# Performance work log

Measured on AMD Instinct MI355X. Metric: run time of the kernel, lower is better.

## Reference

```python
import jax, jax.numpy as jnp
import numpy as np

HID = 128          # hidden_dim
IN_DIM = 256       # input_dim
BOT = 128          # bottleneck_dim
OUT = 4            # output_dim
NQ = 131072        # num query (mesh) points
E = 262144         # num grid->query edges
SEQ = 262144       # grid points (64^3)
B = 1
PE_DIM = 4 * HID   # 512, sincos embed dim over ndim=4


def _linear_params(key, fin, fout):
    k1, k2 = jax.random.split(key)
    lim = 1.0 / np.sqrt(fin)
    w = jax.random.uniform(k1, (fin, fout), minval=-lim, maxval=lim, dtype=jnp.float32)
    b = jax.random.uniform(k2, (fout,), minval=-lim, maxval=lim, dtype=jnp.float32)
    return w, b


def setup_inputs() -> dict:
    key = jax.random.key(0)
    ks = jax.random.split(key, 10)
    x = jax.random.normal(ks[0], (B, SEQ, IN_DIM), dtype=jnp.float32)
    # raw positions in [0, 200) so query_pos/100 - 1 lands in [-1, 1)
    query_pos = jax.random.uniform(ks[1], (NQ, 3), dtype=jnp.float32) * 200.0
    qidx = jnp.sort(jax.random.randint(ks[2], (E,), 0, NQ))          # sorted, as segment_csr assumes
    gidx = jax.random.randint(ks[3], (E,), 0, B * SEQ)
    grid_to_query_edges = jnp.stack([qidx, gidx], axis=1)            # [E, 2] (query_idx, grid_idx)

    msg_w0, msg_b0 = _linear_params(ks[4], IN_DIM + PE_DIM, 512)
    msg_w1, msg_b1 = _linear_params(ks[5], 512, 256)
    msg_w2, msg_b2 = _linear_params(ks[6], 256, BOT)
    pred_w0, pred_b0 = _linear_params(ks[7], BOT, 256)
    pred_w1, pred_b1 = _linear_params(ks[8], 256, OUT)
    return dict(x=x, query_pos=query_pos, grid_to_query_edges=grid_to_query_edges,
                msg_w0=msg_w0, msg_b0=msg_b0, msg_w1=msg_w1, msg_b1=msg_b1,
                msg_w2=msg_w2, msg_b2=msg_b2,
                pred_w0=pred_w0, pred_b0=pred_b0, pred_w1=pred_w1, pred_b1=pred_b1)


def _sincos_embed(coords):
    # coords: [N, 4]; dim=512 -> 128 per coord -> 64 frequencies (no padding needed)
    eff = PE_DIM // 4
    omega = 1.0 / (10000.0 ** (jnp.arange(0, eff, 2, dtype=jnp.float32) / eff))  # [64]
    out = coords[..., None] * omega                                  # [N, 4, 64]
    emb = jnp.concatenate([jnp.sin(out), jnp.cos(out)], axis=-1)     # [N, 4, 128]
    return emb.reshape(coords.shape[0], -1)                          # [N, 512]


def _gelu(x):
    return jax.nn.gelu(x, approximate=False)  # torch nn.GELU default is exact erf


def reference(x, query_pos, grid_to_query_edges,
              msg_w0, msg_b0, msg_w1, msg_b1, msg_w2, msg_b2,
              pred_w0, pred_b0, pred_w1, pred_b1):
    qp = query_pos / 100.0 - 1.0
    ones = jnp.ones((qp.shape[0], 1), dtype=qp.dtype)
    qp = jnp.concatenate([qp, ones], axis=1)                         # [NQ, 4]
    pe = _sincos_embed(qp)                                           # [NQ, 512]

    xf = x.reshape(-1, x.shape[-1])                                  # [B*SEQ, IN_DIM]
    qidx = grid_to_query_edges[:, 0]
    gidx = grid_to_query_edges[:, 1]

    feat = jnp.concatenate([xf[gidx], pe[qidx]], axis=1)             # [E, 768]
    h = _gelu(feat @ msg_w0 + msg_b0)
    h = _gelu(h @ msg_w1 + msg_b1)
    h = h @ msg_w2 + msg_b2                                          # [E, BOT]

    nq = qp.shape[0]
    sums = jax.ops.segment_sum(h, qidx, num_segments=nq)             # [NQ, BOT]
    counts = jax.ops.segment_sum(jnp.ones((h.shape[0],), h.dtype), qidx, num_segments=nq)
    mean = sums / jnp.maximum(counts, 1.0)[:, None]                  # empty segments -> 0 (segment_csr mean)

    out = _gelu(mean @ pred_w0 + pred_b0) @ pred_w1 + pred_b1        # [NQ, OUT]
    return out
```

## Files before the change

kernel.cpp:

```cpp
#include <hip/hip_runtime.h>
#include <cmath>

#define IN_DIM   256
#define H0_DIM   512
#define H1_DIM   256
#define BOT      128
#define NQ_      131072
#define NE_      262144
#define SEQ_     262144
#define QWIN     32768
#define NWIN     (NQ_/QWIN)
#define PE_K     384

static const size_t OFF_XH    = 0;
static const size_t OFF_XL    = 134217728;
static const size_t OFF_Z     = 268435456;
static const size_t OFF_PEH   = 536870912;
static const size_t OFF_PEL   = 562036736;
static const size_t OFF_H2    = 738197504;
static const size_t OFF_W0AH  = 872415232;
static const size_t OFF_W0AL  = 872677376;
static const size_t OFF_W0BH  = 872939520;
static const size_t OFF_W0BL  = 873332736;
static const size_t OFF_W1H   = 873725952;
static const size_t OFF_W1L   = 873988096;
static const size_t OFF_W2H   = 874250240;
static const size_t OFF_W2L   = 874315776;
static const size_t OFF_PW0H  = 874381312;
static const size_t OFF_PW0L  = 874446848;
static const size_t OFF_BCONST= 874512384;
static const size_t OFF_START = 874514432;
static const size_t OFF_MEANH = 0;
static const size_t OFF_MEANL = 33554432;
static const size_t OFF_G1    = 268435456;

typedef __attribute__((ext_vector_type(8))) short bf16x8;
typedef __attribute__((ext_vector_type(4))) float f32x4;

__device__ __forceinline__ float gelu_f(float v) {
    return v * 0.5f * (1.0f + erff(v * 0.7071067811865476f));
}
__device__ __forceinline__ unsigned short f2bf(float f) {
    unsigned int u = __float_as_uint(f);
    unsigned int r = (u + 0x7FFFu + ((u >> 16) & 1u)) >> 16;
    return (unsigned short)r;
}
__device__ __forceinline__ float bf2f(unsigned short h) {
    return __uint_as_float(((unsigned int)h) << 16);
}
__device__ __forceinline__ unsigned int pack2(unsigned short a, unsigned short b) {
    return (unsigned int)a | ((unsigned int)b << 16);
}
__device__ __forceinline__ void stage16(const void* g, void* l) {
    __builtin_amdgcn_global_load_lds(
        (const __attribute__((address_space(1))) unsigned int*)g,
        (__attribute__((address_space(3))) unsigned int*)l,
        16, 0, 0);
}
__device__ __forceinline__ void cvt4(const float4 v, unsigned int* hw, unsigned int* lw) {
    const unsigned short a = f2bf(v.x), b = f2bf(v.y), c = f2bf(v.z), d = f2bf(v.w);
    hw[0] = pack2(a, b); hw[1] = pack2(c, d);
    lw[0] = pack2(f2bf(v.x - bf2f(a)), f2bf(v.y - bf2f(b)));
    lw[1] = pack2(f2bf(v.z - bf2f(c)), f2bf(v.w - bf2f(d)));
}

__global__ __launch_bounds__(256) void conv_x(
    const float* __restrict__ x,
    unsigned short* __restrict__ xH, unsigned short* __restrict__ xL)
{
    const int wv = threadIdx.x >> 6;
    const int l  = threadIdx.x & 63;
    const int row = blockIdx.x * 4 + wv;
    const size_t base = (size_t)row * IN_DIM + l * 4;
    float4 v = *(const float4*)&x[base];
    unsigned short h0 = f2bf(v.x), h1 = f2bf(v.y), h2 = f2bf(v.z), h3 = f2bf(v.w);
    uint2 H, L;
    H.x = pack2(h0, h1); H.y = pack2(h2, h3);
    L.x = pack2(f2bf(v.x - bf2f(h0)), f2bf(v.y - bf2f(h1)));
    L.y = pack2(f2bf(v.z - bf2f(h2)), f2bf(v.w - bf2f(h3)));
    *(uint2*)&xH[base] = H;
    *(uint2*)&xL[base] = L;
}

__global__ __launch_bounds__(256) void conv_w(
    const float* __restrict__ W, unsigned short* __restrict__ WTh,
    unsigned short* __restrict__ WTl, int K, int N)
{
    int idx = blockIdx.x * 256 + threadIdx.x;
    if (idx >= K * N) return;
    int k = idx / N, n = idx % N;
    float v = W[idx];
    unsigned short h = f2bf(v);
    WTh[(size_t)n * K + k] = h;
    WTl[(size_t)n * K + k] = f2bf(v - bf2f(h));
}

__global__ __launch_bounds__(256) void bias_fold(
    const float* __restrict__ w0, const float* __restrict__ b0,
    float* __restrict__ bconst)
{
    int n = blockIdx.x * 256 + threadIdx.x;
    if (n >= H0_DIM) return;
    float s = b0[n];
    for (int j = 0; j < 64; ++j) {
        float om = exp2f((float)j * (-13.287712379549449f / 64.0f));
        s += sinf(om) * w0[(size_t)(640 + j) * H0_DIM + n];
        s += cosf(om) * w0[(size_t)(704 + j) * H0_DIM + n];
    }
    bconst[n] = s;
}

__global__ __launch_bounds__(256) void seg_offsets(
    const int* __restrict__ edges, int* __restrict__ start)
{
    int e = blockIdx.x * 256 + threadIdx.x;
    if (e > NE_) return;
    int qc = (e < NE_) ? edges[2 * e] : NQ_;
    int qp = (e > 0) ? edges[2 * e - 2] : -1;
    for (int q = qp + 1; q <= qc; ++q) start[q] = e;
}

__global__ __launch_bounds__(256) void build_pe(
    const float* __restrict__ qpos, int qbase,
    unsigned short* __restrict__ peH, unsigned short* __restrict__ peL)
{
    const int wv = threadIdx.x >> 6;
    const int l  = threadIdx.x & 63;
    const int i  = blockIdx.x * 4 + wv;
    const int i0 = l * 8;
    if (i0 >= PE_K) return;
    const int q  = qbase + i;
    const size_t base = (size_t)i * PE_K;

    const int cc = i0 >> 7;
    const int j0 = i0 & 127;
    const float cv = qpos[q * 3 + cc] * 0.01f - 1.0f;
    const bool is_sin = (j0 < 64);
    const int jj0 = j0 & 63;
    unsigned int hw[4], lw[4];
    #pragma unroll
    for (int p2 = 0; p2 < 4; ++p2) {
        unsigned short hh[2], ll[2];
        #pragma unroll
        for (int s = 0; s < 2; ++s) {
            int jj = jj0 + p2 * 2 + s;
            float om  = exp2f((float)jj * (-13.287712379549449f / 64.0f));
            float arg = cv * om;
            float v   = is_sin ? __sinf(arg) : __cosf(arg);
            unsigned short h = f2bf(v);
            hh[s] = h; ll[s] = f2bf(v - bf2f(h));
        }
        hw[p2] = pack2(hh[0], hh[1]);
        lw[p2] = pack2(ll[0], ll[1]);
    }
    uint4 H, L;
    H.x = hw[0]; H.y = hw[1]; H.z = hw[2]; H.w = hw[3];
    L.x = lw[0]; L.y = lw[1]; L.z = lw[2]; L.w = lw[3];
    *(uint4*)&peH[base + i0] = H;
    *(uint4*)&peL[base + i0] = L;
}

template <int ACT, int OUT_MODE, int GATHER>
__global__ __launch_bounds__(256) void gemm_mfma(
    const unsigned short* __restrict__ Ah, const unsigned short* __restrict__ Al,
    const unsigned short* __restrict__ Bh, const unsigned short* __restrict__ Bl,
    const float* __restrict__ bias,
    float* __restrict__ Cf, unsigned short* __restrict__ ChO, unsigned short* __restrict__ ClO,
    int M, int K, int N,
    const int* __restrict__ gp, const float* __restrict__ Zw)
{
    __shared__ __align__(16) short lds[4][128][32];

    const int tid = threadIdx.x;
    const int w   = tid >> 6;
    const int l   = tid & 63;
    const int l16 = l & 15;
    const int lq  = l >> 4;
    const int bm  = blockIdx.y * 128;
    const int bn  = blockIdx.x * 128;
    const int wm  = (w & 1) * 64;
    const int wn  = (w >> 1) * 64;

    f32x4 acc[4][4];
    #pragma unroll
    for (int i = 0; i < 4; ++i)
        #pragma unroll
        for (int j = 0; j < 4; ++j)
            acc[i][j] = (f32x4){0.f, 0.f, 0.f, 0.f};

    const int jrow = l >> 2;
    const int jkc  = l & 3;
    const int t0 = w * 2, t1 = t0 + 1;
    const int r0 = t0 * 16 + jrow, r1 = t1 * 16 + jrow;

    size_t arow0, arow1;
    if (GATHER) {
        arow0 = (size_t)gp[2 * (bm + r0) + 1] * K;
        arow1 = (size_t)gp[2 * (bm + r1) + 1] * K;
    } else {
        arow0 = (size_t)(bm + r0) * K;
        arow1 = (size_t)(bm + r1) * K;
    }
    const size_t brow0 = (size_t)(bn + r0) * K;
    const size_t brow1 = (size_t)(bn + r1) * K;
    short* d00 = &lds[0][0][0] + t0 * 512;
    short* d01 = &lds[1][0][0] + t0 * 512;
    short* d02 = &lds[2][0][0] + t0 * 512;
    short* d03 = &lds[3][0][0] + t0 * 512;
    short* d10 = &lds[0][0][0] + t1 * 512;
    short* d11 = &lds[1][0][0] + t1 * 512;
    short* d12 = &lds[2][0][0] + t1 * 512;
    short* d13 = &lds[3][0][0] + t1 * 512;

    for (int k0 = 0; k0 < K; k0 += 32) {
        const int ko = k0 + jkc * 8;
        stage16(Ah + arow0 + ko, d00);
        stage16(Al + arow0 + ko, d01);
        stage16(Bh + brow0 + ko, d02);
        stage16(Bl + brow0 + ko, d03);
        stage16(Ah + arow1 + ko, d10);
        stage16(Al + arow1 + ko, d11);
        stage16(Bh + brow1 + ko, d12);
        stage16(Bl + brow1 + ko, d13);
        __syncthreads();

        bf16x8 ah[4], al[4], bh[4], bl[4];
        #pragma unroll
        for (int i = 0; i < 4; ++i) {
            ah[i] = *(const bf16x8*)&lds[0][wm + i*16 + l16][lq*8];
            al[i] = *(const bf16x8*)&lds[1][wm + i*16 + l16][lq*8];
            bh[i] = *(const bf16x8*)&lds[2][wn + i*16 + l16][lq*8];
            bl[i] = *(const bf16x8*)&lds[3][wn + i*16 + l16][lq*8];
        }
        #pragma unroll
        for (int i = 0; i < 4; ++i)
            #pragma unroll
            for (int j = 0; j < 4; ++j) {
                acc[i][j] = __builtin_amdgcn_mfma_f32_16x16x32_bf16(ah[i], bh[j], acc[i][j], 0, 0, 0);
                acc[i][j] = __builtin_amdgcn_mfma_f32_16x16x32_bf16(ah[i], bl[j], acc[i][j], 0, 0, 0);
                acc[i][j] = __builtin_amdgcn_mfma_f32_16x16x32_bf16(al[i], bh[j], acc[i][j], 0, 0, 0);
            }
        __syncthreads();
    }

    if (OUT_MODE == 0) {
        #pragma unroll
        for (int j = 0; j < 4; ++j) {
            int n = bn + wn + j * 16 + l16;
            float bv = bias[n];
            #pragma unroll
            for (int i = 0; i < 4; ++i) {
                int mrow = bm + wm + i * 16 + lq * 4;
                #pragma unroll
                for (int r = 0; r < 4; ++r) {
                    float v = acc[i][j][r] + bv;
                    if (ACT) v = gelu_f(v);
                    Cf[(size_t)(mrow + r) * N + n] = v;
                }
            }
        }
    }
}

__global__ __launch_bounds__(256, 2) void fused_edge(
    const unsigned short* __restrict__ xHg, const unsigned short* __restrict__ xLg,
    const unsigned short* __restrict__ w0aHg, const unsigned short* __restrict__ w0aLg,
    const unsigned short* __restrict__ w1Hg, const unsigned short* __restrict__ w1Lg,
    const unsigned short* __restrict__ w2Hg, const unsigned short* __restrict__ w2Lg,
    const float* __restrict__ Zg, const float* __restrict__ b1g,
    const float* __restrict__ b2g, const int* __restrict__ gp,
    float* __restrict__ h2g)
{
    extern __shared__ __align__(16) short smem[];
    short* stg = smem;
    short* h0h = smem + 16384;
    short* h0l = smem + 24576;

    const int tid = threadIdx.x;
    const int w   = tid >> 6;
    const int l   = tid & 63;
    const int l16 = l & 15;
    const int lq  = l >> 4;
    const int bm  = blockIdx.x * 64;

    const int wn_p = w * 32;
    const int wn1  = w * 64;

    const int rx = tid >> 2;
    const int ux = tid & 3;
    const size_t xoff = (size_t)gp[2 * (bm + rx) + 1] * IN_DIM + ux * 8;
    const int q_e = gp[2 * (bm + l)];
    float* lbuf = ((float*)stg) + w * 2048;

    short* stgAh  = stg;
    short* stgAl  = stg + 2048;
    short* stgBh  = stg + 4096;
    short* stgBl  = stg + 8192;
    short* stgW1h = stg;
    short* stgW1l = stg + 8192;
    short* stgW2h = stg;
    short* stgW2l = stg + 4096;

    f32x4 h1acc[4][4];
    #pragma unroll
    for (int i = 0; i < 4; ++i)
        #pragma unroll
        for (int j = 0; j < 4; ++j)
            h1acc[i][j] = (f32x4){0.f, 0.f, 0.f, 0.f};

    for (int c = 0; c < 4; ++c) {
        f32x4 acc1[4][2];
        #pragma unroll
        for (int i = 0; i < 4; ++i)
            #pragma unroll
            for (int j = 0; j < 2; ++j)
                acc1[i][j] = (f32x4){0.f, 0.f, 0.f, 0.f};

        {
            const size_t wo = (size_t)(c * 128 + rx) * IN_DIM + ux * 8;
            stage16(xHg + xoff, stgAh + tid * 8);
            stage16(xLg + xoff, stgAl + tid * 8);
            stage16(w0aHg + wo,                      stgBh + tid * 8);
            stage16(w0aLg + wo,                      stgBl + tid * 8);
            stage16(w0aHg + wo + (size_t)64 * IN_DIM, stgBh + 2048 + tid * 8);
            stage16(w0aLg + wo + (size_t)64 * IN_DIM, stgBl + 2048 + tid * 8);
        }
        __syncthreads();
        for (int ks = 0; ks < 8; ++ks) {
            bf16x8 ah[4], al[4], bh[2], bl[2];
            #pragma unroll
            for (int i = 0; i < 4; ++i) {
                const int ro = (i * 16 + l16) * 32 + lq * 8;
                ah[i] = *(const bf16x8*)&stgAh[ro];
                al[i] = *(const bf16x8*)&stgAl[ro];
            }
            #pragma unroll
            for (int j = 0; j < 2; ++j) {
                const int ro = (wn_p + j * 16 + l16) * 32 + lq * 8;
                bh[j] = *(const bf16x8*)&stgBh[ro];
                bl[j] = *(const bf16x8*)&stgBl[ro];
            }
            __syncthreads();
            if (ks < 7) {
                const int ko = (ks + 1) * 32;
                const size_t wo = (size_t)(c * 128 + rx) * IN_DIM + ko + ux * 8;
                stage16(xHg + xoff + ko, stgAh + tid * 8);
                stage16(xLg + xoff + ko, stgAl + tid * 8);
                stage16(w0aHg + wo,                      stgBh + tid * 8);
                stage16(w0aLg + wo,                      stgBl + tid * 8);
                stage16(w0aHg + wo + (size_t)64 * IN_DIM, stgBh + 2048 + tid * 8);
                stage16(w0aLg + wo + (size_t)64 * IN_DIM, stgBl + 2048 + tid * 8);
            }
            #pragma unroll
            for (int i = 0; i < 4; ++i)
                #pragma unroll
                for (int j = 0; j < 2; ++j) {
                    acc1[i][j] = __builtin_amdgcn_mfma_f32_16x16x32_bf16(ah[i], bh[j], acc1[i][j], 0, 0, 0);
                    acc1[i][j] = __builtin_amdgcn_mfma_f32_16x16x32_bf16(ah[i], bl[j], acc1[i][j], 0, 0, 0);
                    acc1[i][j] = __builtin_amdgcn_mfma_f32_16x16x32_bf16(al[i], bh[j], acc1[i][j], 0, 0, 0);
                }
            __syncthreads();
        }

        #pragma unroll
        for (int j = 0; j < 2; ++j)
            #pragma unroll
            for (int i = 0; i < 4; ++i)
                #pragma unroll
                for (int r = 0; r < 4; ++r) {
                    const int rowq = i * 16 + lq * 4 + r;
                    const int u = j * 4 + (l16 >> 2);
                    lbuf[rowq * 32 + (((u ^ (rowq & 7)) << 2) | (l16 & 3))] = acc1[i][j][r];
                }
        __syncthreads();
        {
            const float* zrow = Zg + (size_t)q_e * H0_DIM + c * 128 + wn_p;
            #pragma unroll
            for (int g = 0; g < 2; ++g) {
                unsigned int hw[8], lw[8];
                #pragma unroll
                for (int c2 = 0; c2 < 4; ++c2) {
                    const int cq = g * 4 + c2;
                    float4 v = *(const float4*)&lbuf[l * 32 + ((cq ^ (l & 7)) << 2)];
                    const float4 z = *(const float4*)&zrow[cq * 4];
                    v.x = gelu_f(v.x + z.x); v.y = gelu_f(v.y + z.y);
                    v.z = gelu_f(v.z + z.z); v.w = gelu_f(v.w + z.w);
                    cvt4(v, &hw[c2 * 2], &lw[c2 * 2]);
                }
                const int u0 = (wn_p >> 3) + g * 2;
                const int o0 = l * 128 + (((u0    ) ^ (l & 7)) << 3);
                const int o1 = l * 128 + (((u0 + 1) ^ (l & 7)) << 3);
                uint4 H0, H1, L0, L1;
                H0.x = hw[0]; H0.y = hw[1]; H0.z = hw[2]; H0.w = hw[3];
                H1.x = hw[4]; H1.y = hw[5]; H1.z = hw[6]; H1.w = hw[7];
                L0.x = lw[0]; L0.y = lw[1]; L0.z = lw[2]; L0.w = lw[3];
                L1.x = lw[4]; L1.y = lw[5]; L1.z = lw[6]; L1.w = lw[7];
                *(uint4*)&h0h[o0] = H0; *(uint4*)&h0h[o1] = H1;
                *(uint4*)&h0l[o0] = L0; *(uint4*)&h0l[o1] = L1;
            }
        }
        __syncthreads();

        {
            #pragma unroll
            for (int p = 0; p < 4; ++p) {
                const size_t o = (size_t)(rx + 64 * p) * H0_DIM + c * 128 + ux * 8;
                stage16(w1Hg + o, stgW1h + p * 2048 + tid * 8);
                stage16(w1Lg + o, stgW1l + p * 2048 + tid * 8);
            }
        }
        __syncthreads();
        for (int ks = 0; ks < 4; ++ks) {
            bf16x8 ah[4], al[4], bh[4], bl[4];
            #pragma unroll
            for (int i = 0; i < 4; ++i) {
                const int row = i * 16 + l16;
                const int uo = ((ks * 4 + lq) ^ (row & 7)) << 3;
                ah[i] = *(const bf16x8*)&h0h[row * 128 + uo];
                al[i] = *(const bf16x8*)&h0l[row * 128 + uo];
            }
            #pragma unroll
            for (int j = 0; j < 4; ++j) {
                const int ro = (wn1 + j * 16 + l16) * 32 + lq * 8;
                bh[j] = *(const bf16x8*)&stgW1h[ro];
                bl[j] = *(const bf16x8*)&stgW1l[ro];
            }
            __syncthreads();
            if (ks < 3) {
                #pragma unroll
                for (int p = 0; p < 4; ++p) {
                    const size_t o = (size_t)(rx + 64 * p) * H0_DIM + c * 128 + (ks + 1) * 32 + ux * 8;
                    stage16(w1Hg + o, stgW1h + p * 2048 + tid * 8);
                    stage16(w1Lg + o, stgW1l + p * 2048 + tid * 8);
                }
            }
            #pragma unroll
            for (int i = 0; i < 4; ++i)
                #pragma unroll
                for (int j = 0; j < 4; ++j) {
                    h1acc[i][j] = __builtin_amdgcn_mfma_f32_16x16x32_bf16(ah[i], bh[j], h1acc[i][j], 0, 0, 0);
                    h1acc[i][j] = __builtin_amdgcn_mfma_f32_16x16x32_bf16(ah[i], bl[j], h1acc[i][j], 0, 0, 0);
                    h1acc[i][j] = __builtin_amdgcn_mfma_f32_16x16x32_bf16(al[i], bh[j], h1acc[i][j], 0, 0, 0);
                }
            __syncthreads();
        }
    }

    f32x4 acc2[4][2];
    #pragma unroll
    for (int i = 0; i < 4; ++i)
        #pragma unroll
        for (int j = 0; j < 2; ++j)
            acc2[i][j] = (f32x4){0.f, 0.f, 0.f, 0.f};

    for (int kh = 0; kh < 2; ++kh) {
        const bool my = ((w >> 1) == kh);
        #pragma unroll
        for (int j2 = 0; j2 < 2; ++j2) {
            if (my) {
                #pragma unroll
                for (int jj = 0; jj < 2; ++jj) {
                    const int j = j2 * 2 + jj;
                    const float bv = b1g[wn1 + j * 16 + l16];
                    #pragma unroll
                    for (int i = 0; i < 4; ++i)
                        #pragma unroll
                        for (int r = 0; r < 4; ++r) {
                            const int rowq = i * 16 + lq * 4 + r;
                            const int u = jj * 4 + (l16 >> 2);
                            lbuf[rowq * 32 + (((u ^ (rowq & 7)) << 2) | (l16 & 3))] =
                                gelu_f(h1acc[i][j][r] + bv);
                        }
                }
            }
            __syncthreads();
            if (my) {
                const int colb = (w & 1) * 64 + j2 * 32;
                #pragma unroll
                for (int g = 0; g < 2; ++g) {
                    unsigned int hw[8], lw[8];
                    #pragma unroll
                    for (int c2 = 0; c2 < 4; ++c2) {
                        const int cq = g * 4 + c2;
                        float4 v = *(const float4*)&lbuf[l * 32 + ((cq ^ (l & 7)) << 2)];
                        cvt4(v, &hw[c2 * 2], &lw[c2 * 2]);
                    }
                    const int u0 = ((colb + g * 16) >> 3);
                    const int o0 = l * 128 + (((u0    ) ^ (l & 7)) << 3);
                    const int o1 = l * 128 + (((u0 + 1) ^ (l & 7)) << 3);
                    uint4 H0, H1, L0, L1;
                    H0.x = hw[0]; H0.y = hw[1]; H0.z = hw[2]; H0.w = hw[3];
                    H1.x = hw[4]; H1.y = hw[5]; H1.z = hw[6]; H1.w = hw[7];
                    L0.x = lw[0]; L0.y = lw[1]; L0.z = lw[2]; L0.w = lw[3];
                    L1.x = lw[4]; L1.y = lw[5]; L1.z = lw[6]; L1.w = lw[7];
                    *(uint4*)&h0h[o0] = H0; *(uint4*)&h0h[o1] = H1;
                    *(uint4*)&h0l[o0] = L0; *(uint4*)&h0l[o1] = L1;
                }
            }
            __syncthreads();
        }

        {
            #pragma unroll
            for (int p = 0; p < 2; ++p) {
                const size_t o = (size_t)(rx + 64 * p) * H1_DIM + kh * 128 + ux * 8;
                stage16(w2Hg + o, stgW2h + p * 2048 + tid * 8);
                stage16(w2Lg + o, stgW2l + p * 2048 + tid * 8);
            }
        }
        __syncthreads();
        for (int ks = 0; ks < 4; ++ks) {
            bf16x8 ah[4], al[4], bh[2], bl[2];
            #pragma unroll
            for (int i = 0; i < 4; ++i) {
                const int row = i * 16 + l16;
                const int uo = ((ks * 4 + lq) ^ (row & 7)) << 3;
                ah[i] = *(const bf16x8*)&h0h[row * 128 + uo];
                al[i] = *(const bf16x8*)&h0l[row * 128 + uo];
            }
            #pragma unroll
            for (int j = 0; j < 2; ++j) {
                const int ro = (wn_p + j * 16 + l16) * 32 + lq * 8;
                bh[j] = *(const bf16x8*)&stgW2h[ro];
                bl[j] = *(const bf16x8*)&stgW2l[ro];
            }
            __syncthreads();
            if (ks < 3) {
                #pragma unroll
                for (int p = 0; p < 2; ++p) {
                    const size_t o = (size_t)(rx + 64 * p) * H1_DIM + kh * 128 + (ks + 1) * 32 + ux * 8;
                    stage16(w2Hg + o, stgW2h + p * 2048 + tid * 8);
                    stage16(w2Lg + o, stgW2l + p * 2048 + tid * 8);
                }
            }
            #pragma unroll
            for (int i = 0; i < 4; ++i)
                #pragma unroll
                for (int j = 0; j < 2; ++j) {
                    acc2[i][j] = __builtin_amdgcn_mfma_f32_16x16x32_bf16(ah[i], bh[j], acc2[i][j], 0, 0, 0);
                    acc2[i][j] = __builtin_amdgcn_mfma_f32_16x16x32_bf16(ah[i], bl[j], acc2[i][j], 0, 0, 0);
                    acc2[i][j] = __builtin_amdgcn_mfma_f32_16x16x32_bf16(al[i], bh[j], acc2[i][j], 0, 0, 0);
                }
            __syncthreads();
        }
    }

    #pragma unroll
    for (int j = 0; j < 2; ++j) {
        const int n = wn_p + j * 16 + l16;
        const float bv = b2g[n];
        #pragma unroll
        for (int i = 0; i < 4; ++i) {
            const int er = bm + i * 16 + lq * 4;
            #pragma unroll
            for (int r = 0; r < 4; ++r)
                h2g[(size_t)(er + r) * BOT + n] = acc2[i][j][r] + bv;
        }
    }
}

__global__ __launch_bounds__(256) void seg_mean(
    const int* __restrict__ start, const float* __restrict__ h2,
    unsigned short* __restrict__ mH, unsigned short* __restrict__ mL)
{
    const int t = threadIdx.x;
    const int q = blockIdx.x * 8 + (t >> 5);
    const int quad = t & 31;
    const int s = start[q];
    const int e = start[q + 1];

    float4 acc = make_float4(0.f, 0.f, 0.f, 0.f);
    for (int i = s; i < e; ++i) {
        const float4 v = *(const float4*)&h2[(size_t)i * BOT + quad * 4];
        acc.x += v.x; acc.y += v.y; acc.z += v.z; acc.w += v.w;
    }
    const float inv = 1.0f / (float)((e - s) > 0 ? (e - s) : 1);
    float m0 = acc.x * inv, m1 = acc.y * inv, m2 = acc.z * inv, m3 = acc.w * inv;
    unsigned short h0 = f2bf(m0), h1 = f2bf(m1), h2s = f2bf(m2), h3 = f2bf(m3);
    uint2 H, L;
    H.x = pack2(h0, h1); H.y = pack2(h2s, h3);
    L.x = pack2(f2bf(m0 - bf2f(h0)), f2bf(m1 - bf2f(h1)));
    L.y = pack2(f2bf(m2 - bf2f(h2s)), f2bf(m3 - bf2f(h3)));
    *(uint2*)&mH[(size_t)q * BOT + quad * 4] = H;
    *(uint2*)&mL[(size_t)q * BOT + quad * 4] = L;
}

__global__ __launch_bounds__(256) void pred1_kernel(
    const float* __restrict__ g1, const float* __restrict__ w,
    const float* __restrict__ b, float* __restrict__ out)
{
    const int wave = threadIdx.x >> 6;
    const int lane = threadIdx.x & 63;
    const int row  = blockIdx.x * 4 + wave;

    const float* g = g1 + (size_t)row * 256;
    float a0 = 0, a1 = 0, a2 = 0, a3 = 0;
    #pragma unroll
    for (int i = 0; i < 4; ++i) {
        int k = lane + 64 * i;
        float gv = g[k];
        const float* wr = w + k * 4;
        a0 = fmaf(gv, wr[0], a0);
        a1 = fmaf(gv, wr[1], a1);
        a2 = fmaf(gv, wr[2], a2);
        a3 = fmaf(gv, wr[3], a3);
    }
    #pragma unroll
    for (int off = 32; off > 0; off >>= 1) {
        a0 += __shfl_down(a0, off, 64);
        a1 += __shfl_down(a1, off, 64);
        a2 += __shfl_down(a2, off, 64);
        a3 += __shfl_down(a3, off, 64);
    }
    if (lane == 0) {
        float4 o = {a0 + b[0], a1 + b[1], a2 + b[2], a3 + b[3]};
        *(float4*)&out[(size_t)row * 4] = o;
    }
}

extern "C" void kernel_launch(void* const* d_in, const int* in_sizes, int n_in,
                              void* d_out, int out_size, void* d_ws, size_t ws_size,
                              hipStream_t stream)
{
    const float* x    = (const float*)d_in[0];
    const float* qpos = (const float*)d_in[1];
    const int*   edges= (const int*)  d_in[2];
    const float* w0   = (const float*)d_in[3];
    const float* b0   = (const float*)d_in[4];
    const float* w1   = (const float*)d_in[5];
    const float* b1   = (const float*)d_in[6];
    const float* w2   = (const float*)d_in[7];
    const float* b2   = (const float*)d_in[8];
    const float* pw0  = (const float*)d_in[9];
    const float* pb0  = (const float*)d_in[10];
    const float* pw1  = (const float*)d_in[11];
    const float* pb1  = (const float*)d_in[12];
    float* out = (float*)d_out;

    char* ws = (char*)d_ws;
    unsigned short* xH    = (unsigned short*)(ws + OFF_XH);
    unsigned short* xL    = (unsigned short*)(ws + OFF_XL);
    float*          Z     = (float*)(ws + OFF_Z);
    unsigned short* peH   = (unsigned short*)(ws + OFF_PEH);
    unsigned short* peL   = (unsigned short*)(ws + OFF_PEL);
    float*          h2    = (float*)(ws + OFF_H2);
    unsigned short* w0aH  = (unsigned short*)(ws + OFF_W0AH);
    unsigned short* w0aL  = (unsigned short*)(ws + OFF_W0AL);
    unsigned short* w0bH  = (unsigned short*)(ws + OFF_W0BH);
    unsigned short* w0bL  = (unsigned short*)(ws + OFF_W0BL);
    unsigned short* w1H   = (unsigned short*)(ws + OFF_W1H);
    unsigned short* w1L   = (unsigned short*)(ws + OFF_W1L);
    unsigned short* w2H   = (unsigned short*)(ws + OFF_W2H);
    unsigned short* w2L   = (unsigned short*)(ws + OFF_W2L);
    unsigned short* pw0H  = (unsigned short*)(ws + OFF_PW0H);
    unsigned short* pw0L  = (unsigned short*)(ws + OFF_PW0L);
    float*          bconst= (float*)(ws + OFF_BCONST);
    int*            start = (int*)(ws + OFF_START);
    unsigned short* meanH = (unsigned short*)(ws + OFF_MEANH);
    unsigned short* meanL = (unsigned short*)(ws + OFF_MEANL);
    float*          g1    = (float*)(ws + OFF_G1);

    static bool attr_done = false;
    if (!attr_done) {
        hipFuncSetAttribute(reinterpret_cast<const void*>(&fused_edge),
                            hipFuncAttributeMaxDynamicSharedMemorySize, 65536);
        attr_done = true;
    }

    conv_x<<<SEQ_/4, 256, 0, stream>>>(x, xH, xL);
    conv_w<<<(IN_DIM*H0_DIM + 255)/256, 256, 0, stream>>>(w0, w0aH, w0aL, IN_DIM, H0_DIM);
    conv_w<<<(PE_K*H0_DIM + 255)/256, 256, 0, stream>>>(w0 + (size_t)IN_DIM*H0_DIM, w0bH, w0bL, PE_K, H0_DIM);
    conv_w<<<(H0_DIM*H1_DIM + 255)/256, 256, 0, stream>>>(w1, w1H, w1L, H0_DIM, H1_DIM);
    conv_w<<<(H1_DIM*BOT + 255)/256, 256, 0, stream>>>(w2, w2H, w2L, H1_DIM, BOT);
    conv_w<<<(BOT*H1_DIM + 255)/256, 256, 0, stream>>>(pw0, pw0H, pw0L, BOT, H1_DIM);
    bias_fold<<<2, 256, 0, stream>>>(w0, b0, bconst);
    seg_offsets<<<(NE_ + 1 + 255)/256, 256, 0, stream>>>(edges, start);

    for (int wn = 0; wn < NWIN; ++wn) {
        build_pe<<<QWIN/4, 256, 0, stream>>>(qpos, wn * QWIN, peH, peL);
        gemm_mfma<0, 0, 0><<<dim3(H0_DIM/128, QWIN/128), 256, 0, stream>>>(
            peH, peL, w0bH, w0bL, bconst, Z + (size_t)wn * QWIN * H0_DIM,
            nullptr, nullptr, QWIN, PE_K, H0_DIM, nullptr, nullptr);
    }

    fused_edge<<<NE_/64, 256, 65536, stream>>>(
        xH, xL, w0aH, w0aL, w1H, w1L, w2H, w2L,
        Z, b1, b2, edges, h2);

    seg_mean<<<NQ_/8, 256, 0, stream>>>(start, h2, meanH, meanL);
    gemm_mfma<1, 0, 0><<<dim3(H1_DIM/128, NQ_/128), 256, 0, stream>>>(
        meanH, meanL, pw0H, pw0L, pb0, g1, nullptr, nullptr,
        NQ_, BOT, H1_DIM, nullptr, nullptr);
    pred1_kernel<<<NQ_/4, 256, 0, stream>>>(g1, pw1, pb1, out);
}
```

Measured before the change: 1.580 ms.

## Double-buffer LDS staging with XOR swizzle in GEMM and fused edge kernel

Converts the k-loop staging in gemm_mfma and the first layer of fused_edge to a two-buffer pipeline. Loads for step k+2 are issued while step k computes, and explicit vmcnt/lgkmcnt waits replace full syncthreads. It also XOR-swizzles the LDS column chunk to reduce bank conflicts on the bf16x8 reads. The cost is more LDS (fused_edge dynamic shared memory grows to 80KB), which could reduce occupancy, and the hand-written waitcnt logic is fragile.

```diff
diff --git a/kernel.cpp b/kernel.cpp
--- a/kernel.cpp
+++ b/kernel.cpp
@@ -57,6 +57,11 @@
         (__attribute__((address_space(3))) unsigned int*)l,
         16, 0, 0);
 }
+#define WAITV0 asm volatile("s_waitcnt vmcnt(0)" ::: "memory")
+#define WAITV6 asm volatile("s_waitcnt vmcnt(6)" ::: "memory")
+#define WAITV8 asm volatile("s_waitcnt vmcnt(8)" ::: "memory")
+#define WAITL0 asm volatile("s_waitcnt lgkmcnt(0)" ::: "memory")
+
 __device__ __forceinline__ void cvt4(const float4 v, unsigned int* hw, unsigned int* lw) {
     const unsigned short a = f2bf(v.x), b = f2bf(v.y), c = f2bf(v.z), d = f2bf(v.w);
     hw[0] = pack2(a, b); hw[1] = pack2(c, d);
@@ -169,7 +174,7 @@
     int M, int K, int N,
     const int* __restrict__ gp, const float* __restrict__ Zw)
 {
-    __shared__ __align__(16) short lds[4][128][32];
+    __shared__ __align__(16) short lds[2][4][128][32];
 
     const int tid = threadIdx.x;
     const int w   = tid >> 6;
@@ -190,6 +195,8 @@
 
     const int jrow = l >> 2;
     const int jkc  = l & 3;
+    const int jswz = (jkc ^ (jrow & 3)) * 8;
+    const int rswz = (lq ^ (l16 & 3)) * 8;
     const int t0 = w * 2, t1 = t0 + 1;
     const int r0 = t0 * 16 + jrow, r1 = t1 * 16 + jrow;
 
@@ -203,35 +210,43 @@
     }
     const size_t brow0 = (size_t)(bn + r0) * K;
     const size_t brow1 = (size_t)(bn + r1) * K;
-    short* d00 = &lds[0][0][0] + t0 * 512;
-    short* d01 = &lds[1][0][0] + t0 * 512;
-    short* d02 = &lds[2][0][0] + t0 * 512;
-    short* d03 = &lds[3][0][0] + t0 * 512;
-    short* d10 = &lds[0][0][0] + t1 * 512;
-    short* d11 = &lds[1][0][0] + t1 * 512;
-    short* d12 = &lds[2][0][0] + t1 * 512;
-    short* d13 = &lds[3][0][0] + t1 * 512;
-
-    for (int k0 = 0; k0 < K; k0 += 32) {
-        const int ko = k0 + jkc * 8;
-        stage16(Ah + arow0 + ko, d00);
-        stage16(Al + arow0 + ko, d01);
-        stage16(Bh + brow0 + ko, d02);
-        stage16(Bl + brow0 + ko, d03);
-        stage16(Ah + arow1 + ko, d10);
-        stage16(Al + arow1 + ko, d11);
-        stage16(Bh + brow1 + ko, d12);
-        stage16(Bl + brow1 + ko, d13);
-        __syncthreads();
+
+    const int NK = K >> 5;
+
+    auto stage_set = [&](int k, int cb) {
+        const int ko = (k << 5) + jswz;
+        short* base = &lds[cb][0][0][0];
+        stage16(Ah + arow0 + ko, base + t0 * 512);
+        stage16(Al + arow0 + ko, base + 4096 + t0 * 512);
+        stage16(Bh + brow0 + ko, base + 8192 + t0 * 512);
+        stage16(Bl + brow0 + ko, base + 12288 + t0 * 512);
+        stage16(Ah + arow1 + ko, base + t1 * 512);
+        stage16(Al + arow1 + ko, base + 4096 + t1 * 512);
+        stage16(Bh + brow1 + ko, base + 8192 + t1 * 512);
+        stage16(Bl + brow1 + ko, base + 12288 + t1 * 512);
+    };
+
+    stage_set(0, 0);
+    if (NK > 1) stage_set(1, 1);
+
+    for (int ks = 0; ks < NK; ++ks) {
+        const int cur = ks & 1;
+        if (ks == NK - 1) { WAITV0; } else { WAITV8; }
+        __builtin_amdgcn_s_barrier();
 
         bf16x8 ah[4], al[4], bh[4], bl[4];
         #pragma unroll
         for (int i = 0; i < 4; ++i) {
-            ah[i] = *(const bf16x8*)&lds[0][wm + i*16 + l16][lq*8];
-            al[i] = *(const bf16x8*)&lds[1][wm + i*16 + l16][lq*8];
-            bh[i] = *(const bf16x8*)&lds[2][wn + i*16 + l16][lq*8];
-            bl[i] = *(const bf16x8*)&lds[3][wn + i*16 + l16][lq*8];
-        }
+            ah[i] = *(const bf16x8*)&lds[cur][0][wm + i*16 + l16][rswz];
+            al[i] = *(const bf16x8*)&lds[cur][1][wm + i*16 + l16][rswz];
+            bh[i] = *(const bf16x8*)&lds[cur][2][wn + i*16 + l16][rswz];
+            bl[i] = *(const bf16x8*)&lds[cur][3][wn + i*16 + l16][rswz];
+        }
+        WAITL0;
+        __builtin_amdgcn_sched_barrier(0);
+        __builtin_amdgcn_s_barrier();
+        if (ks + 2 < NK) stage_set(ks + 2, cur);
+
         #pragma unroll
         for (int i = 0; i < 4; ++i)
             #pragma unroll
@@ -240,7 +255,6 @@
                 acc[i][j] = __builtin_amdgcn_mfma_f32_16x16x32_bf16(ah[i], bl[j], acc[i][j], 0, 0, 0);
                 acc[i][j] = __builtin_amdgcn_mfma_f32_16x16x32_bf16(al[i], bh[j], acc[i][j], 0, 0, 0);
             }
-        __syncthreads();
     }
 
     if (OUT_MODE == 0) {
@@ -272,9 +286,8 @@
     float* __restrict__ h2g)
 {
     extern __shared__ __align__(16) short smem[];
-    short* stg = smem;
-    short* h0h = smem + 16384;
-    short* h0l = smem + 24576;
+    short* h0h = smem + 24576;
+    short* h0l = smem + 32768;
 
     const int tid = threadIdx.x;
     const int w   = tid >> 6;
@@ -288,18 +301,11 @@
 
     const int rx = tid >> 2;
     const int ux = tid & 3;
-    const size_t xoff = (size_t)gp[2 * (bm + rx) + 1] * IN_DIM + ux * 8;
+    const int sx = (ux ^ (rx & 3)) * 8;
+    const int rswz = (lq ^ (l16 & 3)) * 8;
+    const size_t xoff = (size_t)gp[2 * (bm + rx) + 1] * IN_DIM + sx;
     const int q_e = gp[2 * (bm + l)];
-    float* lbuf = ((float*)stg) + w * 2048;
-
-    short* stgAh  = stg;
-    short* stgAl  = stg + 2048;
-    short* stgBh  = stg + 4096;
-    short* stgBl  = stg + 8192;
-    short* stgW1h = stg;
-    short* stgW1l = stg + 8192;
-    short* stgW2h = stg;
-    short* stgW2l = stg + 4096;
+    float* lbuf = ((float*)smem) + w * 2048;
 
     f32x4 h1acc[4][4];
     #pragma unroll
@@ -316,41 +322,42 @@
             for (int j = 0; j < 2; ++j)
                 acc1[i][j] = (f32x4){0.f, 0.f, 0.f, 0.f};
 
-        {
-            const size_t wo = (size_t)(c * 128 + rx) * IN_DIM + ux * 8;
-            stage16(xHg + xoff, stgAh + tid * 8);
-            stage16(xLg + xoff, stgAl + tid * 8);
-            stage16(w0aHg + wo,                      stgBh + tid * 8);
-            stage16(w0aLg + wo,                      stgBl + tid * 8);
-            stage16(w0aHg + wo + (size_t)64 * IN_DIM, stgBh + 2048 + tid * 8);
-            stage16(w0aLg + wo + (size_t)64 * IN_DIM, stgBl + 2048 + tid * 8);
-        }
-        __syncthreads();
+        auto stage1 = [&](int k, short* B) {
+            const int ko = k << 5;
+            const size_t wo = (size_t)(c * 128 + rx) * IN_DIM + ko + sx;
+            stage16(xHg + xoff + ko, B + tid * 8);
+            stage16(xLg + xoff + ko, B + 2048 + tid * 8);
+            stage16(w0aHg + wo,                       B + 4096 + tid * 8);
+            stage16(w0aHg + wo + (size_t)64 * IN_DIM, B + 6144 + tid * 8);
+            stage16(w0aLg + wo,                       B + 8192 + tid * 8);
+            stage16(w0aLg + wo + (size_t)64 * IN_DIM, B + 10240 + tid * 8);
+        };
+
+        stage1(0, smem);
+        stage1(1, smem + 12288);
         for (int ks = 0; ks < 8; ++ks) {
+            short* B = (ks & 1) ? (smem + 12288) : smem;
+            if (ks == 7) { WAITV0; } else { WAITV6; }
+            __builtin_amdgcn_s_barrier();
+
             bf16x8 ah[4], al[4], bh[2], bl[2];
             #pragma unroll
             for (int i = 0; i < 4; ++i) {
-                const int ro = (i * 16 + l16) * 32 + lq * 8;
-                ah[i] = *(const bf16x8*)&stgAh[ro];
-                al[i] = *(const bf16x8*)&stgAl[ro];
+                const int ro = (i * 16 + l16) * 32 + rswz;
+                ah[i] = *(const bf16x8*)&B[ro];
+                al[i] = *(const bf16x8*)&B[2048 + ro];
             }
             #pragma unroll
             for (int j = 0; j < 2; ++j) {
-                const int ro = (wn_p + j * 16 + l16) * 32 + lq * 8;
-                bh[j] = *(const bf16x8*)&stgBh[ro];
-                bl[j] = *(const bf16x8*)&stgBl[ro];
-            }
-            __syncthreads();
-            if (ks < 7) {
-                const int ko = (ks + 1) * 32;
-                const size_t wo = (size_t)(c * 128 + rx) * IN_DIM + ko + ux * 8;
-                stage16(xHg + xoff + ko, stgAh + tid * 8);
-                stage16(xLg + xoff + ko, stgAl + tid * 8);
-                stage16(w0aHg + wo,                      stgBh + tid * 8);
-                stage16(w0aLg + wo,                      stgBl + tid * 8);
-                stage16(w0aHg + wo + (size_t)64 * IN_DIM, stgBh + 2048 + tid * 8);
-                stage16(w0aLg + wo + (size_t)64 * IN_DIM, stgBl + 2048 + tid * 8);
-            }
+                const int ro = (wn_p + j * 16 + l16) * 32 + rswz;
+                bh[j] = *(const bf16x8*)&B[4096 + ro];
+                bl[j] = *(const bf16x8*)&B[8192 + ro];
+            }
+            WAITL0;
+            __builtin_amdgcn_sched_barrier(0);
+            __builtin_amdgcn_s_barrier();
+            if (ks < 6) stage1(ks + 2, B);
+
             #pragma unroll
             for (int i = 0; i < 4; ++i)
                 #pragma unroll
@@ -359,8 +366,8 @@
                     acc1[i][j] = __builtin_amdgcn_mfma_f32_16x16x32_bf16(ah[i], bl[j], acc1[i][j], 0, 0, 0);
                     acc1[i][j] = __builtin_amdgcn_mfma_f32_16x16x32_bf16(al[i], bh[j], acc1[i][j], 0, 0, 0);
                 }
-            __syncthreads();
-        }
+        }
+        __syncthreads();
 
         #pragma unroll
         for (int j = 0; j < 2; ++j)
@@ -404,9 +411,9 @@
         {
             #pragma unroll
             for (int p = 0; p < 4; ++p) {
-                const size_t o = (size_t)(rx + 64 * p) * H0_DIM + c * 128 + ux * 8;
-                stage16(w1Hg + o, stgW1h + p * 2048 + tid * 8);
-                stage16(w1Lg + o, stgW1l + p * 2048 + tid * 8);
+                const size_t o = (size_t)(rx + 64 * p) * H0_DIM + c * 128 + sx;
+                stage16(w1Hg + o, smem + p * 2048 + tid * 8);
+                stage16(w1Lg + o, smem + 8192 + p * 2048 + tid * 8);
             }
         }
         __syncthreads();
@@ -421,17 +428,17 @@
             }
             #pragma unroll
             for (int j = 0; j < 4; ++j) {
-                const int ro = (wn1 + j * 16 + l16) * 32 + lq * 8;
-                bh[j] = *(const bf16x8*)&stgW1h[ro];
-                bl[j] = *(const bf16x8*)&stgW1l[ro];
+                const int ro = (wn1 + j * 16 + l16) * 32 + rswz;
+                bh[j] = *(const bf16x8*)&smem[ro];
+                bl[j] = *(const bf16x8*)&smem[8192 + ro];
             }
             __syncthreads();
             if (ks < 3) {
                 #pragma unroll
                 for (int p = 0; p < 4; ++p) {
-                    const size_t o = (size_t)(rx + 64 * p) * H0_DIM + c * 128 + (ks + 1) * 32 + ux * 8;
-                    stage16(w1Hg + o, stgW1h + p * 2048 + tid * 8);
-                    stage16(w1Lg + o, stgW1l + p * 2048 + tid * 8);
+                    const size_t o = (size_t)(rx + 64 * p) * H0_DIM + c * 128 + (ks + 1) * 32 + sx;
+                    stage16(w1Hg + o, smem + p * 2048 + tid * 8);
+                    stage16(w1Lg + o, smem + 8192 + p * 2048 + tid * 8);
                 }
             }
             #pragma unroll
@@ -503,9 +510,9 @@
         {
             #pragma unroll
             for (int p = 0; p < 2; ++p) {
-                const size_t o = (size_t)(rx + 64 * p) * H1_DIM + kh * 128 + ux * 8;
-                stage16(w2Hg + o, stgW2h + p * 2048 + tid * 8);
-                stage16(w2Lg + o, stgW2l + p * 2048 + tid * 8);
+                const size_t o = (size_t)(rx + 64 * p) * H1_DIM + kh * 128 + sx;
+                stage16(w2Hg + o, smem + p * 2048 + tid * 8);
+                stage16(w2Lg + o, smem + 4096 + p * 2048 + tid * 8);
             }
         }
         __syncthreads();
@@ -520,17 +527,17 @@
             }
             #pragma unroll
             for (int j = 0; j < 2; ++j) {
-                const int ro = (wn_p + j * 16 + l16) * 32 + lq * 8;
-                bh[j] = *(const bf16x8*)&stgW2h[ro];
-                bl[j] = *(const bf16x8*)&stgW2l[ro];
+                const int ro = (wn_p + j * 16 + l16) * 32 + rswz;
+                bh[j] = *(const bf16x8*)&smem[ro];
+                bl[j] = *(const bf16x8*)&smem[4096 + ro];
             }
             __syncthreads();
             if (ks < 3) {
                 #pragma unroll
                 for (int p = 0; p < 2; ++p) {
-                    const size_t o = (size_t)(rx + 64 * p) * H1_DIM + kh * 128 + (ks + 1) * 32 + ux * 8;
-                    stage16(w2Hg + o, stgW2h + p * 2048 + tid * 8);
-                    stage16(w2Lg + o, stgW2l + p * 2048 + tid * 8);
+                    const size_t o = (size_t)(rx + 64 * p) * H1_DIM + kh * 128 + (ks + 1) * 32 + sx;
+                    stage16(w2Hg + o, smem + p * 2048 + tid * 8);
+                    stage16(w2Lg + o, smem + 4096 + p * 2048 + tid * 8);
                 }
             }
             #pragma unroll
@@ -663,7 +670,7 @@
     static bool attr_done = false;
     if (!attr_done) {
         hipFuncSetAttribute(reinterpret_cast<const void*>(&fused_edge),
-                            hipFuncAttributeMaxDynamicSharedMemorySize, 65536);
+                            hipFuncAttributeMaxDynamicSharedMemorySize, 81920);
         attr_done = true;
     }
 
@@ -683,7 +690,7 @@
             nullptr, nullptr, QWIN, PE_K, H0_DIM, nullptr, nullptr);
     }
 
-    fused_edge<<<NE_/64, 256, 65536, stream>>>(
+    fused_edge<<<NE_/64, 256, 81920, stream>>>(
         xH, xL, w0aH, w0aL, w1H, w1L, w2H, w2L,
         Z, b1, b2, edges, h2);
 
```

After: 1.850 ms. +17.1%, slower.

## Double-buffer LDS staging in the MFMA GEMM kernel

Applied to the files above, without the earlier changes.

Moves the gemm_mfma tiles from static shared memory to a 64KB dynamic buffer split into two stages. The next K-slice is staged while MFMAs run on the current one, aiming to hide global load latency and drop one barrier per iteration. Both launches and the function attributes are updated for the larger shared allocation. The cost is double the LDS per block, which can lower occupancy. These GEMMs (the PE projection and the prediction layer) are likely a small share of total time next to fused_edge.

```diff
diff --git a/kernel.cpp b/kernel.cpp
--- a/kernel.cpp
+++ b/kernel.cpp
@@ -169,7 +169,7 @@
     int M, int K, int N,
     const int* __restrict__ gp, const float* __restrict__ Zw)
 {
-    __shared__ __align__(16) short lds[4][128][32];
+    extern __shared__ __align__(16) short gsm[];
 
     const int tid = threadIdx.x;
     const int w   = tid >> 6;
@@ -203,34 +203,39 @@
     }
     const size_t brow0 = (size_t)(bn + r0) * K;
     const size_t brow1 = (size_t)(bn + r1) * K;
-    short* d00 = &lds[0][0][0] + t0 * 512;
-    short* d01 = &lds[1][0][0] + t0 * 512;
-    short* d02 = &lds[2][0][0] + t0 * 512;
-    short* d03 = &lds[3][0][0] + t0 * 512;
-    short* d10 = &lds[0][0][0] + t1 * 512;
-    short* d11 = &lds[1][0][0] + t1 * 512;
-    short* d12 = &lds[2][0][0] + t1 * 512;
-    short* d13 = &lds[3][0][0] + t1 * 512;
-
-    for (int k0 = 0; k0 < K; k0 += 32) {
-        const int ko = k0 + jkc * 8;
-        stage16(Ah + arow0 + ko, d00);
-        stage16(Al + arow0 + ko, d01);
-        stage16(Bh + brow0 + ko, d02);
-        stage16(Bl + brow0 + ko, d03);
-        stage16(Ah + arow1 + ko, d10);
-        stage16(Al + arow1 + ko, d11);
-        stage16(Bh + brow1 + ko, d12);
-        stage16(Bl + brow1 + ko, d13);
-        __syncthreads();
-
+
+    auto stg = [&](int k, int cb) {
+        const int ko = (k << 5) + jkc * 8;
+        short* B = gsm + cb * 16384;
+        stage16(Ah + arow0 + ko, B + t0 * 512);
+        stage16(Al + arow0 + ko, B + 4096 + t0 * 512);
+        stage16(Bh + brow0 + ko, B + 8192 + t0 * 512);
+        stage16(Bl + brow0 + ko, B + 12288 + t0 * 512);
+        stage16(Ah + arow1 + ko, B + t1 * 512);
+        stage16(Al + arow1 + ko, B + 4096 + t1 * 512);
+        stage16(Bh + brow1 + ko, B + 8192 + t1 * 512);
+        stage16(Bl + brow1 + ko, B + 12288 + t1 * 512);
+    };
+
+    const int NK = K >> 5;
+    stg(0, 0);
+    __syncthreads();
+
+    #pragma unroll 1
+    for (int ks = 0; ks < NK; ++ks) {
+        const int cb = ks & 1;
+        if (ks + 1 < NK) stg(ks + 1, cb ^ 1);
+
+        const short* B = gsm + cb * 16384;
         bf16x8 ah[4], al[4], bh[4], bl[4];
         #pragma unroll
         for (int i = 0; i < 4; ++i) {
-            ah[i] = *(const bf16x8*)&lds[0][wm + i*16 + l16][lq*8];
-            al[i] = *(const bf16x8*)&lds[1][wm + i*16 + l16][lq*8];
-            bh[i] = *(const bf16x8*)&lds[2][wn + i*16 + l16][lq*8];
-            bl[i] = *(const bf16x8*)&lds[3][wn + i*16 + l16][lq*8];
+            const int roA = (wm + i * 16 + l16) * 32 + lq * 8;
+            const int roB = (wn + i * 16 + l16) * 32 + lq * 8;
+            ah[i] = *(const bf16x8*)&B[roA];
+            al[i] = *(const bf16x8*)&B[4096 + roA];
+            bh[i] = *(const bf16x8*)&B[8192 + roB];
+            bl[i] = *(const bf16x8*)&B[12288 + roB];
         }
         #pragma unroll
         for (int i = 0; i < 4; ++i)
@@ -664,6 +669,10 @@
     if (!attr_done) {
         hipFuncSetAttribute(reinterpret_cast<const void*>(&fused_edge),
                             hipFuncAttributeMaxDynamicSharedMemorySize, 65536);
+        hipFuncSetAttribute(reinterpret_cast<const void*>(&gemm_mfma<0, 0, 0>),
+                            hipFuncAttributeMaxDynamicSharedMemorySize, 65536);
+        hipFuncSetAttribute(reinterpret_cast<const void*>(&gemm_mfma<1, 0, 0>),
+                            hipFuncAttributeMaxDynamicSharedMemorySize, 65536);
         attr_done = true;
     }
 
@@ -678,7 +687,7 @@
 
     for (int wn = 0; wn < NWIN; ++wn) {
         build_pe<<<QWIN/4, 256, 0, stream>>>(qpos, wn * QWIN, peH, peL);
-        gemm_mfma<0, 0, 0><<<dim3(H0_DIM/128, QWIN/128), 256, 0, stream>>>(
+        gemm_mfma<0, 0, 0><<<dim3(H0_DIM/128, QWIN/128), 256, 65536, stream>>>(
             peH, peL, w0bH, w0bL, bconst, Z + (size_t)wn * QWIN * H0_DIM,
             nullptr, nullptr, QWIN, PE_K, H0_DIM, nullptr, nullptr);
     }
@@ -688,7 +697,7 @@
         Z, b1, b2, edges, h2);
 
     seg_mean<<<NQ_/8, 256, 0, stream>>>(start, h2, meanH, meanL);
-    gemm_mfma<1, 0, 0><<<dim3(H1_DIM/128, NQ_/128), 256, 0, stream>>>(
+    gemm_mfma<1, 0, 0><<<dim3(H1_DIM/128, NQ_/128), 256, 65536, stream>>>(
         meanH, meanL, pw0H, pw0L, pb0, g1, nullptr, nullptr,
         NQ_, BOT, H1_DIM, nullptr, nullptr);
     pred1_kernel<<<NQ_/4, 256, 0, stream>>>(g1, pw1, pb1, out);
```

New measurement: 1.619 ms. 2.5% more time.
